# Kernel optimization log

Hardware: AMD Instinct MI355X
Metric: run time of the kernel (lower is better)

## Reference

```python
import jax, jax.numpy as jnp
import numpy as np

B, T = 64, 2048
ENC, DEC = 512, 512
KQ, VD = 256, 256
NEG_SLOPE = 0.2


def _leaky(x):
    return jnp.where(x >= 0, x, NEG_SLOPE * x)


def setup_inputs() -> dict:
    key = jax.random.key(0)
    ks = jax.random.split(key, 9)
    s = 0.02
    return {
        "decoder_feat": jax.random.normal(ks[0], (B, DEC), dtype=jnp.float32),
        "encoder_feat": jax.random.normal(ks[1], (B, T, ENC), dtype=jnp.float32),
        "Wq": jax.random.normal(ks[2], (DEC, KQ), dtype=jnp.float32) * s,
        "bq": jnp.zeros((KQ,), dtype=jnp.float32),
        "Wk": jax.random.normal(ks[3], (ENC, KQ), dtype=jnp.float32) * s,
        "bk": jnp.zeros((KQ,), dtype=jnp.float32),
        "Wv": jax.random.normal(ks[4], (ENC, VD), dtype=jnp.float32) * s,
        "bv": jnp.zeros((VD,), dtype=jnp.float32),
        "seq_len": jax.random.randint(ks[5], (B,), 1, T + 1, dtype=jnp.int32),
    }


def reference(decoder_feat, encoder_feat, Wq, bq, Wk, bk, Wv, bv, seq_len):
    # projections + LeakyReLU(0.2)
    query = _leaky(decoder_feat @ Wq + bq)                              # [B, KQ]
    key_p = _leaky(jnp.einsum('bte,ek->btk', encoder_feat, Wk) + bk)    # [B, T, KQ]
    value = _leaky(jnp.einsum('bte,ev->btv', encoder_feat, Wv) + bv)    # [B, T, VD]
    # single-query scores over T encoder frames
    energy = jnp.einsum('bk,btk->bt', query, key_p)                     # [B, T]
    score = jax.nn.softmax(energy, axis=1)
    # ragged length mask (vectorized arange-compare), then renormalize
    mask = (jnp.arange(T)[None, :] < seq_len[:, None]).astype(score.dtype)
    score = score * mask
    score = score / jnp.sum(score, axis=1, keepdims=True)
    context = jnp.einsum('bt,btv->bv', score, value)                    # [B, VD]
    return score, context
```

## Files before the change

kernel.cpp:

```cpp
#include <hip/hip_runtime.h>
#include <hip/hip_bf16.h>

constexpr int B_SZ  = 64;
constexpr int T_SZ  = 2048;
constexpr int E_SZ  = 512;
constexpr int N_SZ  = 512;
constexpr int KQ_SZ = 256;
constexpr int VD_SZ = 256;
constexpr float NEG_SLOPE = 0.2f;

typedef __bf16 bf16_t;
typedef __bf16 bf16x8 __attribute__((ext_vector_type(8)));
typedef __bf16 bf16x4 __attribute__((ext_vector_type(4)));
typedef float  f32x4  __attribute__((ext_vector_type(4)));

__device__ __forceinline__ float leaky(float x) { return x >= 0.f ? x : NEG_SLOPE * x; }

__global__ void prep_kernel(const float* __restrict__ Wk, const float* __restrict__ Wv,
                            const float* __restrict__ bk, const float* __restrict__ bv,
                            bf16_t* __restrict__ Wt, float* __restrict__ bcat)
{
    int g  = blockIdx.x * 256 + threadIdx.x;
    int n  = g >> 7;
    int e0 = (g & 127) * 4;
    const float* src = (n < KQ_SZ) ? (Wk + n) : (Wv + (n - KQ_SZ));
    bf16x4 h;
#pragma unroll
    for (int j = 0; j < 4; ++j) h[j] = (bf16_t)src[(size_t)(e0 + j) * KQ_SZ];
    *reinterpret_cast<bf16x4*>(Wt + (size_t)n * E_SZ + e0) = h;
    if (g < N_SZ) bcat[g] = (g < KQ_SZ) ? bk[g] : bv[g - KQ_SZ];
}

__global__ void query_kernel(const float* __restrict__ dec, const float* __restrict__ Wq,
                             const float* __restrict__ bq, float* __restrict__ q)
{
    int b = blockIdx.x, k = threadIdx.x;
    __shared__ float ds[E_SZ];
    ds[k]       = dec[b * E_SZ + k];
    ds[k + 256] = dec[b * E_SZ + k + 256];
    __syncthreads();
    float acc = bq[k];
#pragma unroll 8
    for (int e = 0; e < E_SZ; ++e) acc += ds[e] * Wq[(size_t)e * KQ_SZ + k];
    q[b * KQ_SZ + k] = leaky(acc);
}

constexpr int BM = 128, BN = 128, BK = 64;

__global__ __launch_bounds__(256, 2) void gemm_kv_kernel(
    const float* __restrict__ enc, const bf16_t* __restrict__ Wt,
    const float* __restrict__ bcat, const int* __restrict__ seq_len,
    bf16_t* __restrict__ KV)
{
    const int bid = blockIdx.x;
    const int nb = bid & 3;
    const int tb = (bid >> 2) & 15;
    const int b  = bid >> 6;
    const int len = seq_len[b];
    if (tb * BM >= len) return;

    const int tid  = threadIdx.x;
    const int lane = tid & 63;
    const int wid  = tid >> 6;
    const int wm   = wid >> 1;
    const int wn   = wid & 1;

    __shared__ bf16_t As[BM][BK];
    __shared__ bf16_t Bs[BN][BK];
    __shared__ float  biasS[BN];

    if (tid < BN) biasS[tid] = bcat[nb * BN + tid];

    const int t0 = tb * BM;
    const size_t encBase = ((size_t)b * T_SZ + t0) * E_SZ;

    float4 aReg[8];
    uint4  bReg[4];

    auto loadA = [&](int ks) {
        const int k0 = ks * BK;
#pragma unroll
        for (int i = 0; i < 8; ++i) {
            int c = tid + i * 256;
            int row = c >> 4, c4 = c & 15;
            aReg[i] = *reinterpret_cast<const float4*>(
                enc + encBase + (size_t)row * E_SZ + k0 + c4 * 4);
        }
    };
    auto loadB = [&](int ks) {
        const int k0 = ks * BK;
#pragma unroll
        for (int i = 0; i < 4; ++i) {
            int c = tid + i * 256;
            int nrow = c >> 3, kc = (c & 7) * 8;
            bReg[i] = *reinterpret_cast<const uint4*>(
                Wt + (size_t)(nb * BN + nrow) * E_SZ + k0 + kc);
        }
    };
    auto writeA = [&]() {
#pragma unroll
        for (int i = 0; i < 8; ++i) {
            int c = tid + i * 256;
            int row = c >> 4, c4 = c & 15;
            bf16x4 h;
            h[0] = (bf16_t)aReg[i].x; h[1] = (bf16_t)aReg[i].y;
            h[2] = (bf16_t)aReg[i].z; h[3] = (bf16_t)aReg[i].w;
            *reinterpret_cast<bf16x4*>(&As[row][c4 * 4]) = h;
        }
    };
    auto writeB = [&]() {
#pragma unroll
        for (int i = 0; i < 4; ++i) {
            int c = tid + i * 256;
            int nrow = c >> 3, kc = (c & 7) * 8;
            *reinterpret_cast<uint4*>(&Bs[nrow][kc]) = bReg[i];
        }
    };

    f32x4 acc[4][4];
#pragma unroll
    for (int m = 0; m < 4; ++m)
#pragma unroll
        for (int n = 0; n < 4; ++n) acc[m][n] = (f32x4){0.f, 0.f, 0.f, 0.f};

    loadA(0); loadB(0);
    for (int ks = 0; ks < E_SZ / BK; ++ks) {
        writeA(); writeB();
        __syncthreads();
        if (ks < E_SZ / BK - 1) { loadA(ks + 1); loadB(ks + 1); }
#pragma unroll
        for (int s = 0; s < 2; ++s) {
            bf16x8 af[4], bfr[4];
#pragma unroll
            for (int m = 0; m < 4; ++m)
                af[m] = *reinterpret_cast<const bf16x8*>(
                    &As[wm * 64 + m * 16 + (lane & 15)][s * 32 + (lane >> 4) * 8]);
#pragma unroll
            for (int n = 0; n < 4; ++n)
                bfr[n] = *reinterpret_cast<const bf16x8*>(
                    &Bs[wn * 64 + n * 16 + (lane & 15)][s * 32 + (lane >> 4) * 8]);
#pragma unroll
            for (int m = 0; m < 4; ++m)
#pragma unroll
                for (int n = 0; n < 4; ++n)
                    acc[m][n] = __builtin_amdgcn_mfma_f32_16x16x32_bf16(
                        af[m], bfr[n], acc[m][n], 0, 0, 0);
        }
        __syncthreads();
    }

#pragma unroll
    for (int m = 0; m < 4; ++m) {
#pragma unroll
        for (int n = 0; n < 4; ++n) {
            int col  = wn * 64 + n * 16 + (lane & 15);
            float bias = biasS[col];
            int rowq = wm * 64 + m * 16 + ((lane >> 4) * 4);
#pragma unroll
            for (int r = 0; r < 4; ++r) {
                float v = leaky(acc[m][n][r] + bias);
                int t = t0 + rowq + r;
                KV[((size_t)b * T_SZ + t) * N_SZ + nb * BN + col] = (bf16_t)v;
            }
        }
    }
}

__global__ void energy_kernel(const bf16_t* __restrict__ KV, const float* __restrict__ q,
                              const int* __restrict__ seq_len, float* __restrict__ energy)
{
    int b = blockIdx.y, c = blockIdx.x, tid = threadIdx.x;
    __shared__ float qs[KQ_SZ];
    qs[tid] = q[b * KQ_SZ + tid];
    __syncthreads();
    int t = c * 256 + tid;
    int len = seq_len[b];
    if (t >= len) return;
    const bf16_t* row = KV + ((size_t)b * T_SZ + t) * N_SZ;
    float acc = 0.f;
#pragma unroll 4
    for (int k = 0; k < KQ_SZ; k += 8) {
        bf16x8 v = *reinterpret_cast<const bf16x8*>(row + k);
#pragma unroll
        for (int j = 0; j < 8; ++j) acc += (float)v[j] * qs[k + j];
    }
    energy[b * T_SZ + t] = acc;
}

__global__ void softmax_kernel(const float* __restrict__ energy, const int* __restrict__ seq_len,
                               float* __restrict__ score)
{
    const int b = blockIdx.x, tid = threadIdx.x;
    const int lane = tid & 63, wid = tid >> 6;
    const int len = seq_len[b];
    float e[8];
    float m = -1e30f;
#pragma unroll
    for (int i = 0; i < 8; ++i) {
        int t = i * 256 + tid;
        e[i] = (t < len) ? energy[b * T_SZ + t] : -1e30f;
        m = fmaxf(m, e[i]);
    }
#pragma unroll
    for (int o = 32; o > 0; o >>= 1) m = fmaxf(m, __shfl_xor(m, o));
    __shared__ float rm[4], rs[4];
    if (lane == 0) rm[wid] = m;
    __syncthreads();
    m = fmaxf(fmaxf(rm[0], rm[1]), fmaxf(rm[2], rm[3]));
    float p[8], s = 0.f;
#pragma unroll
    for (int i = 0; i < 8; ++i) { p[i] = __expf(e[i] - m); s += p[i]; }
#pragma unroll
    for (int o = 32; o > 0; o >>= 1) s += __shfl_xor(s, o);
    if (lane == 0) rs[wid] = s;
    __syncthreads();
    s = rs[0] + rs[1] + rs[2] + rs[3];
    float inv = 1.0f / s;
#pragma unroll
    for (int i = 0; i < 8; ++i) {
        int t = i * 256 + tid;
        score[b * T_SZ + t] = p[i] * inv;
    }
}

__global__ void ctx_partial_kernel(const bf16_t* __restrict__ KV, const float* __restrict__ score,
                                   const int* __restrict__ seq_len, float* __restrict__ part)
{
    int b = blockIdx.y, c = blockIdx.x, v = threadIdx.x;
    int len = seq_len[b];
    float acc = 0.f;
    if (c * 256 < len) {
        __shared__ float ss[256];
        ss[v] = score[b * T_SZ + c * 256 + v];
        __syncthreads();
        int tlim = min(256, len - c * 256);
        const bf16_t* base = KV + ((size_t)b * T_SZ + c * 256) * N_SZ + KQ_SZ + v;
#pragma unroll 8
        for (int tt = 0; tt < tlim; ++tt) acc += ss[tt] * (float)base[(size_t)tt * N_SZ];
    }
    part[(b * 8 + c) * VD_SZ + v] = acc;
}

__global__ void ctx_reduce_kernel(const float* __restrict__ part, float* __restrict__ ctx)
{
    int b = blockIdx.x, v = threadIdx.x;
    float s = 0.f;
#pragma unroll
    for (int c = 0; c < 8; ++c) s += part[(b * 8 + c) * VD_SZ + v];
    ctx[b * VD_SZ + v] = s;
}

extern "C" void kernel_launch(void* const* d_in, const int* in_sizes, int n_in,
                              void* d_out, int out_size, void* d_ws, size_t ws_size,
                              hipStream_t stream)
{
    const float* dec = (const float*)d_in[0];
    const float* enc = (const float*)d_in[1];
    const float* Wq  = (const float*)d_in[2];
    const float* bq  = (const float*)d_in[3];
    const float* Wk  = (const float*)d_in[4];
    const float* bk  = (const float*)d_in[5];
    const float* Wv  = (const float*)d_in[6];
    const float* bv  = (const float*)d_in[7];
    const int* seq_len = (const int*)d_in[8];

    float* out   = (float*)d_out;
    float* score = out;
    float* ctx   = out + B_SZ * T_SZ;

    char* ws = (char*)d_ws;
    size_t off = 0;
    auto alloc = [&](size_t bytes) { size_t o = off; off += (bytes + 255) & ~(size_t)255; return o; };
    bf16_t* Wt     = (bf16_t*)(ws + alloc((size_t)N_SZ * E_SZ * sizeof(bf16_t)));
    float*  bcat   = (float* )(ws + alloc((size_t)N_SZ * sizeof(float)));
    float*  q      = (float* )(ws + alloc((size_t)B_SZ * KQ_SZ * sizeof(float)));
    float*  energy = (float* )(ws + alloc((size_t)B_SZ * T_SZ * sizeof(float)));
    float*  part   = (float* )(ws + alloc((size_t)B_SZ * 8 * VD_SZ * sizeof(float)));
    bf16_t* KV     = (bf16_t*)(ws + alloc((size_t)B_SZ * T_SZ * N_SZ * sizeof(bf16_t)));

    prep_kernel       <<<256, 256, 0, stream>>>(Wk, Wv, bk, bv, Wt, bcat);
    query_kernel      <<<B_SZ, 256, 0, stream>>>(dec, Wq, bq, q);
    gemm_kv_kernel    <<<B_SZ * (T_SZ / BM) * (N_SZ / BN), 256, 0, stream>>>(enc, Wt, bcat, seq_len, KV);
    energy_kernel     <<<dim3(T_SZ / 256, B_SZ), 256, 0, stream>>>(KV, q, seq_len, energy);
    softmax_kernel    <<<B_SZ, 256, 0, stream>>>(energy, seq_len, score);
    ctx_partial_kernel<<<dim3(8, B_SZ), 256, 0, stream>>>(KV, score, seq_len, part);
    ctx_reduce_kernel <<<B_SZ, 256, 0, stream>>>(part, ctx);
}
```

Baseline: 587.8 us.

## Fuse energy dot into KV GEMM epilogue, swizzle LDS, remap blocks per XCD

The key projection is no longer written to global memory. The GEMM epilogue for the key column tiles computes leaky(K)·q directly, reduces it across lanes with shuffles, and atomically adds partial energies into a zeroed buffer. The value tiles are staged through LDS and written as coalesced 16-byte rows into a V-only buffer. The change also adds an XOR swizzle on the A/B LDS tiles to avoid bank conflicts, remaps block IDs so tiles of the same batch share an XCD, and raises the occupancy hint to 3. In exchange it adds a memset and float atomics, which make the energy summation order nondeterministic.

```diff
diff --git a/kernel.cpp b/kernel.cpp
--- a/kernel.cpp
+++ b/kernel.cpp
@@ -4,7 +4,6 @@
 constexpr int B_SZ  = 64;
 constexpr int T_SZ  = 2048;
 constexpr int E_SZ  = 512;
-constexpr int N_SZ  = 512;
 constexpr int KQ_SZ = 256;
 constexpr int VD_SZ = 256;
 constexpr float NEG_SLOPE = 0.2f;
@@ -28,7 +27,7 @@
 #pragma unroll
     for (int j = 0; j < 4; ++j) h[j] = (bf16_t)src[(size_t)(e0 + j) * KQ_SZ];
     *reinterpret_cast<bf16x4*>(Wt + (size_t)n * E_SZ + e0) = h;
-    if (g < N_SZ) bcat[g] = (g < KQ_SZ) ? bk[g] : bv[g - KQ_SZ];
+    if (g < 512) bcat[g] = (g < KQ_SZ) ? bk[g] : bv[g - KQ_SZ];
 }
 
 __global__ void query_kernel(const float* __restrict__ dec, const float* __restrict__ Wq,
@@ -47,15 +46,26 @@
 
 constexpr int BM = 128, BN = 128, BK = 64;
 
-__global__ __launch_bounds__(256, 2) void gemm_kv_kernel(
+constexpr int CS_STRIDE = 272;
+constexpr int SMEM_BYTES = BM * CS_STRIDE;
+
+__device__ __forceinline__ int swz(int row, int cb) {
+    return row * 128 + (cb ^ ((row & 7) << 4));
+}
+
+__global__ __launch_bounds__(256, 3) void gemm_kv_kernel(
     const float* __restrict__ enc, const bf16_t* __restrict__ Wt,
-    const float* __restrict__ bcat, const int* __restrict__ seq_len,
-    bf16_t* __restrict__ KV)
-{
-    const int bid = blockIdx.x;
-    const int nb = bid & 3;
-    const int tb = (bid >> 2) & 15;
-    const int b  = bid >> 6;
+    const float* __restrict__ bcat, const float* __restrict__ q,
+    const int* __restrict__ seq_len,
+    bf16_t* __restrict__ Vbuf, float* __restrict__ energy)
+{
+    const int w   = blockIdx.x;
+    const int xcd = w & 7;
+    const int s0  = w >> 3;
+    const int nb  = s0 & 3;
+    const int g   = (s0 >> 2) * 8 + xcd;
+    const int b   = g & 63;
+    const int tb  = g >> 6;
     const int len = seq_len[b];
     if (tb * BM >= len) return;
 
@@ -65,11 +75,14 @@
     const int wm   = wid >> 1;
     const int wn   = wid & 1;
 
-    __shared__ bf16_t As[BM][BK];
-    __shared__ bf16_t Bs[BN][BK];
-    __shared__ float  biasS[BN];
-
-    if (tid < BN) biasS[tid] = bcat[nb * BN + tid];
+    __shared__ __align__(16) char smem[SMEM_BYTES];
+    __shared__ float biasS[128];
+    __shared__ float qs[128];
+
+    if (tid < 128) {
+        biasS[tid] = bcat[nb * 128 + tid];
+        if (nb < 2) qs[tid] = q[b * KQ_SZ + nb * 128 + tid];
+    }
 
     const int t0 = tb * BM;
     const size_t encBase = ((size_t)b * T_SZ + t0) * E_SZ;
@@ -101,19 +114,19 @@
 #pragma unroll
         for (int i = 0; i < 8; ++i) {
             int c = tid + i * 256;
-            int row = c >> 4, c4 = c & 15;
+            int row = c >> 4, cb = (c & 15) * 8;
             bf16x4 h;
             h[0] = (bf16_t)aReg[i].x; h[1] = (bf16_t)aReg[i].y;
             h[2] = (bf16_t)aReg[i].z; h[3] = (bf16_t)aReg[i].w;
-            *reinterpret_cast<bf16x4*>(&As[row][c4 * 4]) = h;
+            *reinterpret_cast<bf16x4*>(smem + swz(row, cb)) = h;
         }
     };
     auto writeB = [&]() {
 #pragma unroll
         for (int i = 0; i < 4; ++i) {
             int c = tid + i * 256;
-            int nrow = c >> 3, kc = (c & 7) * 8;
-            *reinterpret_cast<uint4*>(&Bs[nrow][kc]) = bReg[i];
+            int nrow = c >> 3, cb = (c & 7) * 16;
+            *reinterpret_cast<uint4*>(smem + 16384 + swz(nrow, cb)) = bReg[i];
         }
     };
 
@@ -131,14 +144,15 @@
 #pragma unroll
         for (int s = 0; s < 2; ++s) {
             bf16x8 af[4], bfr[4];
+            const int cb = s * 64 + (lane >> 4) * 16;
 #pragma unroll
             for (int m = 0; m < 4; ++m)
                 af[m] = *reinterpret_cast<const bf16x8*>(
-                    &As[wm * 64 + m * 16 + (lane & 15)][s * 32 + (lane >> 4) * 8]);
+                    smem + swz(wm * 64 + m * 16 + (lane & 15), cb));
 #pragma unroll
             for (int n = 0; n < 4; ++n)
                 bfr[n] = *reinterpret_cast<const bf16x8*>(
-                    &Bs[wn * 64 + n * 16 + (lane & 15)][s * 32 + (lane >> 4) * 8]);
+                    smem + 16384 + swz(wn * 64 + n * 16 + (lane & 15), cb));
 #pragma unroll
             for (int m = 0; m < 4; ++m)
 #pragma unroll
@@ -149,42 +163,53 @@
         __syncthreads();
     }
 
-#pragma unroll
-    for (int m = 0; m < 4; ++m) {
-#pragma unroll
-        for (int n = 0; n < 4; ++n) {
-            int col  = wn * 64 + n * 16 + (lane & 15);
-            float bias = biasS[col];
-            int rowq = wm * 64 + m * 16 + ((lane >> 4) * 4);
+    if (nb < 2) {
+        float myval = 0.f;
+#pragma unroll
+        for (int m = 0; m < 4; ++m) {
 #pragma unroll
             for (int r = 0; r < 4; ++r) {
-                float v = leaky(acc[m][n][r] + bias);
-                int t = t0 + rowq + r;
-                KV[((size_t)b * T_SZ + t) * N_SZ + nb * BN + col] = (bf16_t)v;
+                float v = 0.f;
+#pragma unroll
+                for (int n = 0; n < 4; ++n) {
+                    int col = wn * 64 + n * 16 + (lane & 15);
+                    v += leaky(acc[m][n][r] + biasS[col]) * qs[col];
+                }
+#pragma unroll
+                for (int o = 1; o < 16; o <<= 1) v += __shfl_xor(v, o);
+                if ((lane & 15) == (m * 4 + r)) myval = v;
             }
         }
-    }
-}
-
-__global__ void energy_kernel(const bf16_t* __restrict__ KV, const float* __restrict__ q,
-                              const int* __restrict__ seq_len, float* __restrict__ energy)
-{
-    int b = blockIdx.y, c = blockIdx.x, tid = threadIdx.x;
-    __shared__ float qs[KQ_SZ];
-    qs[tid] = q[b * KQ_SZ + tid];
-    __syncthreads();
-    int t = c * 256 + tid;
-    int len = seq_len[b];
-    if (t >= len) return;
-    const bf16_t* row = KV + ((size_t)b * T_SZ + t) * N_SZ;
-    float acc = 0.f;
-#pragma unroll 4
-    for (int k = 0; k < KQ_SZ; k += 8) {
-        bf16x8 v = *reinterpret_cast<const bf16x8*>(row + k);
-#pragma unroll
-        for (int j = 0; j < 8; ++j) acc += (float)v[j] * qs[k + j];
-    }
-    energy[b * T_SZ + t] = acc;
+        int mm = (lane & 15) >> 2, rr = lane & 3;
+        int row = wm * 64 + mm * 16 + (lane >> 4) * 4 + rr;
+        atomicAdd(&energy[b * T_SZ + t0 + row], myval);
+    } else {
+#pragma unroll
+        for (int m = 0; m < 4; ++m) {
+#pragma unroll
+            for (int n = 0; n < 4; ++n) {
+                int col = wn * 64 + n * 16 + (lane & 15);
+                float bias = biasS[col];
+#pragma unroll
+                for (int r = 0; r < 4; ++r) {
+                    int row = wm * 64 + m * 16 + (lane >> 4) * 4 + r;
+                    *reinterpret_cast<bf16_t*>(smem + row * CS_STRIDE + (col * 2)) =
+                        (bf16_t)leaky(acc[m][n][r] + bias);
+                }
+            }
+        }
+        __syncthreads();
+        const int row  = tid >> 1;
+        const int half = tid & 1;
+        const size_t vbase = ((size_t)b * T_SZ + t0 + row) * VD_SZ
+                             + (nb - 2) * 128 + half * 64;
+#pragma unroll
+        for (int i = 0; i < 8; ++i) {
+            bf16x8 hv = *reinterpret_cast<const bf16x8*>(
+                smem + row * CS_STRIDE + half * 128 + i * 16);
+            *reinterpret_cast<bf16x8*>(Vbuf + vbase + i * 8) = hv;
+        }
+    }
 }
 
 __global__ void softmax_kernel(const float* __restrict__ energy, const int* __restrict__ seq_len,
@@ -223,7 +248,7 @@
     }
 }
 
-__global__ void ctx_partial_kernel(const bf16_t* __restrict__ KV, const float* __restrict__ score,
+__global__ void ctx_partial_kernel(const bf16_t* __restrict__ Vbuf, const float* __restrict__ score,
                                    const int* __restrict__ seq_len, float* __restrict__ part)
 {
     int b = blockIdx.y, c = blockIdx.x, v = threadIdx.x;
@@ -234,9 +259,9 @@
         ss[v] = score[b * T_SZ + c * 256 + v];
         __syncthreads();
         int tlim = min(256, len - c * 256);
-        const bf16_t* base = KV + ((size_t)b * T_SZ + c * 256) * N_SZ + KQ_SZ + v;
+        const bf16_t* base = Vbuf + ((size_t)b * T_SZ + c * 256) * VD_SZ + v;
 #pragma unroll 8
-        for (int tt = 0; tt < tlim; ++tt) acc += ss[tt] * (float)base[(size_t)tt * N_SZ];
+        for (int tt = 0; tt < tlim; ++tt) acc += ss[tt] * (float)base[(size_t)tt * VD_SZ];
     }
     part[(b * 8 + c) * VD_SZ + v] = acc;
 }
@@ -271,18 +296,19 @@
     char* ws = (char*)d_ws;
     size_t off = 0;
     auto alloc = [&](size_t bytes) { size_t o = off; off += (bytes + 255) & ~(size_t)255; return o; };
-    bf16_t* Wt     = (bf16_t*)(ws + alloc((size_t)N_SZ * E_SZ * sizeof(bf16_t)));
-    float*  bcat   = (float* )(ws + alloc((size_t)N_SZ * sizeof(float)));
+    bf16_t* Wt     = (bf16_t*)(ws + alloc((size_t)512 * E_SZ * sizeof(bf16_t)));
+    float*  bcat   = (float* )(ws + alloc((size_t)512 * sizeof(float)));
     float*  q      = (float* )(ws + alloc((size_t)B_SZ * KQ_SZ * sizeof(float)));
     float*  energy = (float* )(ws + alloc((size_t)B_SZ * T_SZ * sizeof(float)));
     float*  part   = (float* )(ws + alloc((size_t)B_SZ * 8 * VD_SZ * sizeof(float)));
-    bf16_t* KV     = (bf16_t*)(ws + alloc((size_t)B_SZ * T_SZ * N_SZ * sizeof(bf16_t)));
+    bf16_t* Vbuf   = (bf16_t*)(ws + alloc((size_t)B_SZ * T_SZ * VD_SZ * sizeof(bf16_t)));
+
+    hipMemsetAsync(energy, 0, (size_t)B_SZ * T_SZ * sizeof(float), stream);
 
     prep_kernel       <<<256, 256, 0, stream>>>(Wk, Wv, bk, bv, Wt, bcat);
     query_kernel      <<<B_SZ, 256, 0, stream>>>(dec, Wq, bq, q);
-    gemm_kv_kernel    <<<B_SZ * (T_SZ / BM) * (N_SZ / BN), 256, 0, stream>>>(enc, Wt, bcat, seq_len, KV);
-    energy_kernel     <<<dim3(T_SZ / 256, B_SZ), 256, 0, stream>>>(KV, q, seq_len, energy);
+    gemm_kv_kernel    <<<B_SZ * 16 * 4, 256, 0, stream>>>(enc, Wt, bcat, q, seq_len, Vbuf, energy);
     softmax_kernel    <<<B_SZ, 256, 0, stream>>>(energy, seq_len, score);
-    ctx_partial_kernel<<<dim3(8, B_SZ), 256, 0, stream>>>(KV, score, seq_len, part);
+    ctx_partial_kernel<<<dim3(8, B_SZ), 256, 0, stream>>>(Vbuf, score, seq_len, part);
     ctx_reduce_kernel <<<B_SZ, 256, 0, stream>>>(part, ctx);
 }
```

New measurement: 539.8 us. 1.09x faster.
